# Kernel tuning notes

Measured on AMD Instinct MI355X. Metric: run time of the kernel, lower is better.

The kernel has to match this reference:

```python
import jax, jax.numpy as jnp
import numpy as np

RADIUS = 3
SIGMA = 2.0
T_STEPS = 30


def _gauss_kernel():
    i = jnp.arange(-RADIUS, RADIUS + 1, dtype=jnp.float32)
    w = jnp.exp(-0.5 * (i / SIGMA) ** 2)
    return w / w.sum()


def _gauss_axis(x, w, axis):
    # scipy mode='reflect' == numpy pad mode='symmetric'
    pad = [(0, 0)] * x.ndim
    pad[axis] = (RADIUS, RADIUS)
    xp = jnp.pad(x, pad, mode='symmetric')
    n = x.shape[axis]
    out = w[0] * jax.lax.slice_in_dim(xp, 0, n, axis=axis)
    for k in range(1, 2 * RADIUS + 1):
        out = out + w[k] * jax.lax.slice_in_dim(xp, k, k + n, axis=axis)
    return out


def _dog(x):
    # scipy gaussian_filter with scalar sigma filters EVERY axis (incl. batch, channel).
    # sigma2=0 axis filters are skipped by scipy -> blurred2 == x.
    w = _gauss_kernel()
    g = x
    for ax in range(x.ndim):
        g = _gauss_axis(g, w, ax)
    return jnp.abs(g - x)


def _conv(x, w):
    return jax.lax.conv_general_dilated(
        x, w, window_strides=(1, 1), padding='VALID',
        dimension_numbers=('NCHW', 'OIHW', 'NCHW'))


def _maxpool2(x, pad):
    return jax.lax.reduce_window(
        x, -jnp.inf, jax.lax.max, (1, 1, 2, 2), (1, 1, 2, 2),
        [(0, 0), (0, 0), (pad, pad), (pad, pad)])


def setup_inputs() -> dict:
    key = jax.random.key(0)
    kx, k1, k2, k3 = jax.random.split(key, 4)
    x = jax.random.uniform(kx, (4096, 1, 28, 28), dtype=jnp.float32)
    # model constructor takes abs() of all conv weights
    w1 = jnp.abs(jax.random.normal(k1, (4, 1, 3, 3), dtype=jnp.float32) / 3.0)
    w2 = jnp.abs(jax.random.normal(k2, (4, 4, 3, 3), dtype=jnp.float32) / 6.0)
    w3 = jnp.abs(jax.random.normal(k3, (1, 4, 3, 3), dtype=jnp.float32) / 6.0)
    return {'x': x, 'w1': w1, 'w2': w2, 'w3': w3}


def reference(x, w1, w2, w3):
    x = x.reshape(-1, 1, 28, 28)
    n = x.shape[0]
    dt = x.dtype
    # DoG preproc + global-max normalization (input is constant across timesteps,
    # so computing it once is mathematically identical to the per-step recompute)
    d = _dog(x)
    d = d / d.max()

    def step(carry, _):
        v1, v2, v3, v4, pred = carry
        # IFNode(4.5): integrate, fire, hard reset to 0
        v1 = v1 + d
        s1 = (v1 >= 4.5).astype(dt)
        v1 = jnp.where(s1 > 0, 0.0, v1)
        # conv1 -> IFNode(4.5) -> maxpool2
        v2 = v2 + _conv(s1, w1)                 # [n,4,26,26]
        s2 = (v2 >= 4.5).astype(dt)
        v2 = jnp.where(s2 > 0, 0.0, v2)
        p1 = _maxpool2(s2, 0)                   # [n,4,13,13]
        # conv2 -> IFNode(1.0) -> maxpool2(pad=1)
        v3 = v3 + _conv(p1, w2)                 # [n,4,11,11]
        s3 = (v3 >= 1.0).astype(dt)
        v3 = jnp.where(s3 > 0, 0.0, v3)
        p2 = _maxpool2(s3, 1)                   # [n,4,6,6]
        # conv3 -> LIFNode(tau=2, v_th=1.0, decay_input=True, hard reset)
        c3 = _conv(p2, w3)                      # [n,1,4,4]
        v4 = v4 + (c3 - v4) / 2.0
        s4 = (v4 >= 1.0).astype(dt)
        v4 = jnp.where(s4 > 0, 0.0, v4)
        return (v1, v2, v3, v4, pred + s4), None

    z = lambda s: jnp.zeros(s, dt)
    carry0 = (z((n, 1, 28, 28)), z((n, 4, 26, 26)), z((n, 4, 11, 11)),
              z((n, 1, 4, 4)), z((n, 1, 4, 4)))
    (v1, v2, v3, v4, pred), _ = jax.lax.scan(step, carry0, None, length=T_STEPS)
    return (pred / T_STEPS).reshape(-1, 4, 4)
```

## Files before the change

kernel.cpp:

```cpp
#include <hip/hip_runtime.h>
#include <math.h>

#define HW 784
#define TSTEPS 30
#define TCHUNK 10

struct GaussW { float w[7]; };

__device__ __forceinline__ float fadd(float a, float b) { return __fadd_rn(a, b); }
__device__ __forceinline__ float fmul(float a, float b) { return __fmul_rn(a, b); }
__device__ __forceinline__ float fsub(float a, float b) { return __fsub_rn(a, b); }

#if defined(__has_builtin)
#  if __has_builtin(__builtin_amdgcn_ubfe)
#    define UBFE(x, o, w) __builtin_amdgcn_ubfe((unsigned)(x), (unsigned)(o), (unsigned)(w))
#  endif
#endif
#ifndef UBFE
#  define UBFE(x, o, w) (((unsigned)(x) >> (o)) & ((1u << (w)) - 1u))
#endif

#define WFENCE() asm volatile("s_waitcnt lgkmcnt(0)" ::: "memory")

__device__ __forceinline__ int refl(int i, int n) {
    if (i < 0) return -i - 1;
    if (i >= n) return 2 * n - 1 - i;
    return i;
}

__device__ void dog_sample(const float* __restrict__ x, int b, int nbatch,
                           const GaussW gw, float* g, float* t,
                           float* dout, int tid) {
    for (int p = tid; p < HW; p += 256) {
        float acc = fmul(gw.w[0], x[(size_t)refl(b - 3, nbatch) * HW + p]);
        #pragma unroll
        for (int k = 1; k < 7; ++k)
            acc = fadd(acc, fmul(gw.w[k], x[(size_t)refl(b - 3 + k, nbatch) * HW + p]));
        float h = fmul(gw.w[0], acc);
        #pragma unroll
        for (int k = 1; k < 7; ++k)
            h = fadd(h, fmul(gw.w[k], acc));
        g[p] = h;
    }
    __syncthreads();
    for (int p = tid; p < HW; p += 256) {
        int i = p / 28, j = p - (p / 28) * 28;
        float acc = fmul(gw.w[0], g[refl(i - 3, 28) * 28 + j]);
        #pragma unroll
        for (int k = 1; k < 7; ++k)
            acc = fadd(acc, fmul(gw.w[k], g[refl(i - 3 + k, 28) * 28 + j]));
        t[p] = acc;
    }
    __syncthreads();
    for (int p = tid; p < HW; p += 256) {
        int i = p / 28, j = p - (p / 28) * 28;
        float acc = fmul(gw.w[0], t[i * 28 + refl(j - 3, 28)]);
        #pragma unroll
        for (int k = 1; k < 7; ++k)
            acc = fadd(acc, fmul(gw.w[k], t[i * 28 + refl(j - 3 + k, 28)]));
        dout[p] = fabsf(fsub(acc, x[(size_t)b * HW + p]));
    }
    __syncthreads();
}

__global__ void init_kernel(unsigned int* dmax) { *dmax = 0u; }

template<bool CACHE>
__global__ __launch_bounds__(256) void dmax_kernel(const float* __restrict__ x,
                                                   int nbatch, GaussW gw,
                                                   unsigned int* __restrict__ dmax,
                                                   float* __restrict__ dcache) {
    __shared__ float gS[4][HW];
    __shared__ float tS[4][HW];
    int tid = threadIdx.x;
    int lane = tid & 63, wv = tid >> 6;
    int b = blockIdx.x * 4 + wv;
    int bs = b < nbatch ? b : nbatch - 1;
    float* g = gS[wv];
    float* t = tS[wv];
    const float* xb = x + (size_t)bs * HW;
    const float* xr[7];
    #pragma unroll
    for (int k = 0; k < 7; ++k)
        xr[k] = x + (size_t)refl(bs - 3 + k, nbatch) * HW;

    for (int r = 0; r < 13; ++r) {
        int p = (r << 6) + lane;
        if (p < HW) {
            float acc = fmul(gw.w[0], xr[0][p]);
            #pragma unroll
            for (int k = 1; k < 7; ++k)
                acc = fadd(acc, fmul(gw.w[k], xr[k][p]));
            float h = fmul(gw.w[0], acc);
            #pragma unroll
            for (int k = 1; k < 7; ++k)
                h = fadd(h, fmul(gw.w[k], acc));
            g[p] = h;
        }
    }
    WFENCE();
    for (int r = 0; r < 13; ++r) {
        int p = (r << 6) + lane;
        if (p < HW) {
            int i = p / 28, j = p - (p / 28) * 28;
            float acc = fmul(gw.w[0], g[refl(i - 3, 28) * 28 + j]);
            #pragma unroll
            for (int k = 1; k < 7; ++k)
                acc = fadd(acc, fmul(gw.w[k], g[refl(i - 3 + k, 28) * 28 + j]));
            t[p] = acc;
        }
    }
    WFENCE();
    float mx = 0.f;
    for (int r = 0; r < 13; ++r) {
        int p = (r << 6) + lane;
        if (p < HW) {
            int i = p / 28, j = p - (p / 28) * 28;
            float acc = fmul(gw.w[0], t[i * 28 + refl(j - 3, 28)]);
            #pragma unroll
            for (int k = 1; k < 7; ++k)
                acc = fadd(acc, fmul(gw.w[k], t[i * 28 + refl(j - 3 + k, 28)]));
            float d = fabsf(fsub(acc, xb[p]));
            if (CACHE) dcache[(size_t)bs * HW + p] = d;
            mx = fmaxf(mx, d);
        }
    }
    #pragma unroll
    for (int off = 32; off; off >>= 1) mx = fmaxf(mx, __shfl_down(mx, off, 64));
    if (lane == 0) atomicMax(dmax, __float_as_uint(mx));
}

template<bool CACHE>
__global__ __launch_bounds__(256, 6) void sim_kernel(const float* __restrict__ x,
        int nbatch,
        const float* __restrict__ w1g, const float* __restrict__ w2g,
        const float* __restrict__ w3g, GaussW gw,
        const unsigned int* __restrict__ dmaxp,
        const float* __restrict__ dcache,
        float* __restrict__ out) {
    __shared__ __align__(16) float4 lut[512];
    __shared__ __align__(8)  float2 lut2[768];
    __shared__ float lut3[96];
    __shared__ float wts[216];
    __shared__ unsigned s1m[TCHUNK * 28];
    __shared__ unsigned p1m[TCHUNK * 52];
    __shared__ unsigned p2m[TCHUNK * 24];

    int tid = threadIdx.x;
    int b = blockIdx.x;
    if (b >= nbatch) b = nbatch - 1;

    if (tid < 36)  wts[tid]       = w1g[tid];
    if (tid < 144) wts[36 + tid]  = w2g[tid];
    if (tid < 36)  wts[180 + tid] = w3g[tid];

    float dmaxv = __uint_as_float(*dmaxp);
    float dnr[4];
    if (CACHE) {
        const float* dcb = dcache + (size_t)b * HW;
        #pragma unroll
        for (int k = 0; k < 4; ++k) {
            int p = tid + (k << 8);
            dnr[k] = (p < HW) ? __fdiv_rn(dcb[p], dmaxv) : 0.f;
        }
    } else {
        float* scr = (float*)lut;
        float* dnbuf = (float*)s1m;
        dog_sample(x, b, nbatch, gw, scr, scr + HW, dnbuf, tid);
        #pragma unroll
        for (int k = 0; k < 4; ++k) {
            int p = tid + (k << 8);
            dnr[k] = (p < HW) ? __fdiv_rn(dnbuf[p], dmaxv) : 0.f;
        }
    }
    __syncthreads();

    for (int e = tid; e < 512; e += 256) {
        float a0 = 0.f, a1 = 0.f, a2 = 0.f, a3 = 0.f;
        #pragma unroll
        for (int k = 0; k < 9; ++k) {
            bool bit = (e >> k) & 1;
            a0 = fadd(a0, bit ? wts[k]      : 0.0f);
            a1 = fadd(a1, bit ? wts[9 + k]  : 0.0f);
            a2 = fadd(a2, bit ? wts[18 + k] : 0.0f);
            a3 = fadd(a3, bit ? wts[27 + k] : 0.0f);
        }
        lut[e] = make_float4(a0, a1, a2, a3);
    }
    for (int e = tid; e < 768; e += 256) {
        int rowIdx = e >> 4, idx = e & 15;
        int cout = rowIdx / 12, rem = rowIdx - cout * 12;
        int ic = rem / 3, ki = rem - ic * 3;
        const float* wb = &wts[36 + cout * 36 + ic * 9 + ki * 3];
        float xx = 0.f, yy = 0.f;
        #pragma unroll
        for (int kk = 0; kk < 3; ++kk) {
            xx = fadd(xx, ((idx >> kk) & 1) ? wb[kk] : 0.0f);
            yy = fadd(yy, ((idx >> (kk + 1)) & 1) ? wb[kk] : 0.0f);
        }
        lut2[e] = make_float2(xx, yy);
    }
    if (tid < 96) {
        int ric = tid >> 3, idx = tid & 7;
        int ic = ric / 3, ki = ric - ic * 3;
        const float* wb = &wts[180 + ic * 9 + ki * 3];
        float xx = 0.f;
        #pragma unroll
        for (int kk = 0; kk < 3; ++kk)
            xx = fadd(xx, ((idx >> kk) & 1) ? wb[kk] : 0.0f);
        lut3[tid] = xx;
    }
    #pragma unroll
    for (int j = 0; j < 5; ++j) {
        int idx = tid + (j << 8);
        if (idx < TCHUNK * 104) {
            if (idx < 280) s1m[idx] = 0u;
            else if (idx < 800) p1m[idx - 280] = 0u;
            else p2m[idx - 800] = 0u;
        }
    }
    __syncthreads();

    int l1w_[4]; unsigned l1b_[4];
    #pragma unroll
    for (int k = 0; k < 4; ++k) {
        int e = tid + (k << 8); if (e >= HW) e = 0;
        int rw = e / 28;
        l1w_[k] = rw; l1b_[k] = 1u << (e - rw * 28);
    }
    bool okq = tid < 169;
    int qq1 = okq ? tid : 0;
    int pi1 = qq1 / 13, pj1 = qq1 - pi1 * 13;
    int sr1 = 2 * pi1; unsigned sh1 = (unsigned)(2 * pj1);
    unsigned pb1 = 1u << (pj1 + 1);
    bool hasB = tid >= 248;
    int i2cA, lb2A, p2wA; unsigned js2A, b20A, b21A;
    int i2cB, lb2B, p2wB; unsigned js2B, b20B, b21B;
    {
        int m = tid;
        int row = m / 6, sub = m - row * 6;
        int j0 = (sub < 5) ? 2 * sub : 10;
        int c = row / 11, i2 = row - c * 11;
        i2cA = i2; js2A = (unsigned)(j0 + 1); lb2A = c * 192;
        p2wA = c * 6 + ((i2 + 1) >> 1);
        b20A = 1u << (j0 >> 1);
        b21A = (sub < 5) ? (2u << (j0 >> 1)) : 0u;
        m = hasB ? 256 + (tid - 248) : 0;
        row = m / 6; sub = m - row * 6;
        j0 = (sub < 5) ? 2 * sub : 10;
        c = row / 11; i2 = row - c * 11;
        i2cB = i2; js2B = (unsigned)(j0 + 1); lb2B = c * 192;
        p2wB = c * 6 + ((i2 + 1) >> 1);
        b20B = 1u << (j0 >> 1);
        b21B = (sub < 5) ? (2u << (j0 >> 1)) : 0u;
    }
    int rr3 = (tid >> 2) & 3, cc3 = tid & 3;

    float v2q[16] = {};
    float v3A[2] = {0.f, 0.f}, v3B[2] = {0.f, 0.f};
    float v1m[4] = {};
    float v4 = 0.f, pred = 0.f;

    const float* lutf = (const float*)lut;
    (void)lutf;

    #pragma unroll 1
    for (int c = 0; c < TSTEPS / TCHUNK; ++c) {
        #pragma unroll 1
        for (int tt = 0; tt < TCHUNK; ++tt) {
            unsigned* s1 = s1m + tt * 28;
            #pragma unroll
            for (int k = 0; k < 4; ++k) {
                if (k < 3 || tid < 16) {
                    float v = fadd(v1m[k], dnr[k]);
                    bool spk = v >= 4.5f;
                    v1m[k] = spk ? 0.f : v;
                    if (spk) atomicOr(&s1[l1w_[k]], l1b_[k]);
                }
            }
        }
        __syncthreads();

        if (okq) {
            #pragma unroll 1
            for (int tt = 0; tt < TCHUNK; ++tt) {
                const unsigned* s1 = s1m + tt * 28;
                unsigned m0 = s1[sr1], m1 = s1[sr1 + 1], m2 = s1[sr1 + 2], m3 = s1[sr1 + 3];
                unsigned a = UBFE(m0, sh1, 4), bq = UBFE(m1, sh1, 4),
                         cq = UBFE(m2, sh1, 4), dq = UBFE(m3, sh1, 4);
                unsigned a7 = a & 7u, b7 = bq & 7u, c7 = cq & 7u, d7 = dq & 7u;
                unsigned a1 = a >> 1, b1 = bq >> 1, c1 = cq >> 1, d1 = dq >> 1;
                unsigned p00 = a7 | (b7 << 3) | (c7 << 6);
                unsigned p01 = a1 | (b1 << 3) | (c1 << 6);
                unsigned p10 = b7 | (c7 << 3) | (d7 << 6);
                unsigned p11 = b1 | (c1 << 3) | (d1 << 6);
                float4 e00 = lut[p00], e01 = lut[p01], e10 = lut[p10], e11 = lut[p11];
                unsigned cb0 = 0, cb1 = 0, cb2 = 0, cb3 = 0;
                #define C1U(E, ci) { float v; bool s; \
                    v = fadd(v2q[(ci)*4+0], E.x); s = v>=4.5f; v2q[(ci)*4+0] = s?0.f:v; cb0 |= (unsigned)s; \
                    v = fadd(v2q[(ci)*4+1], E.y); s = v>=4.5f; v2q[(ci)*4+1] = s?0.f:v; cb1 |= (unsigned)s; \
                    v = fadd(v2q[(ci)*4+2], E.z); s = v>=4.5f; v2q[(ci)*4+2] = s?0.f:v; cb2 |= (unsigned)s; \
                    v = fadd(v2q[(ci)*4+3], E.w); s = v>=4.5f; v2q[(ci)*4+3] = s?0.f:v; cb3 |= (unsigned)s; }
                C1U(e00, 0) C1U(e01, 1) C1U(e10, 2) C1U(e11, 3)
                #undef C1U
                unsigned* p1 = p1m + tt * 52;
                if (cb0) atomicOr(&p1[pi1],      pb1);
                if (cb1) atomicOr(&p1[13 + pi1], pb1);
                if (cb2) atomicOr(&p1[26 + pi1], pb1);
                if (cb3) atomicOr(&p1[39 + pi1], pb1);
            }
        } else {
            #pragma unroll
            for (int j = 0; j < 3; ++j) {
                int idx = (tid - 169) + 87 * j;
                if (idx < TCHUNK * 24) p2m[idx] = 0u;
            }
        }
        __syncthreads();

        #pragma unroll 1
        for (int tt = 0; tt < TCHUNK; ++tt) {
            const unsigned* p1 = p1m + tt * 52;
            unsigned* p2 = p2m + tt * 24;
            float accA = 0.f, accB = 0.f;
            #pragma unroll
            for (int ic = 0; ic < 4; ++ic)
                #pragma unroll
                for (int ki = 0; ki < 3; ++ki) {
                    unsigned row = p1[ic * 13 + i2cA + ki];
                    unsigned idx = UBFE(row, js2A, 4);
                    float2 e = lut2[lb2A + (ic * 3 + ki) * 16 + idx];
                    accA = fadd(accA, e.x);
                    accB = fadd(accB, e.y);
                }
            float va = fadd(v3A[0], accA);
            float vb = fadd(v3A[1], accB);
            bool sa = va >= 1.0f, sb = vb >= 1.0f;
            v3A[0] = sa ? 0.f : va; v3A[1] = sb ? 0.f : vb;
            unsigned orm = (sa ? b20A : 0u) | (sb ? b21A : 0u);
            if (orm) atomicOr(&p2[p2wA], orm);
        }
        if (hasB) {
            #pragma unroll 1
            for (int tt = 0; tt < TCHUNK; ++tt) {
                const unsigned* p1 = p1m + tt * 52;
                unsigned* p2 = p2m + tt * 24;
                float accA = 0.f, accB = 0.f;
                #pragma unroll
                for (int ic = 0; ic < 4; ++ic)
                    #pragma unroll
                    for (int ki = 0; ki < 3; ++ki) {
                        unsigned row = p1[ic * 13 + i2cB + ki];
                        unsigned idx = UBFE(row, js2B, 4);
                        float2 e = lut2[lb2B + (ic * 3 + ki) * 16 + idx];
                        accA = fadd(accA, e.x);
                        accB = fadd(accB, e.y);
                    }
                float va = fadd(v3B[0], accA);
                float vb = fadd(v3B[1], accB);
                bool sa = va >= 1.0f, sb = vb >= 1.0f;
                v3B[0] = sa ? 0.f : va; v3B[1] = sb ? 0.f : vb;
                unsigned orm = (sa ? b20B : 0u) | (sb ? b21B : 0u);
                if (orm) atomicOr(&p2[p2wB], orm);
            }
        }
        __syncthreads();

        if (tid < 16) {
            #pragma unroll 1
            for (int tt = 0; tt < TCHUNK; ++tt) {
                const unsigned* p2 = p2m + tt * 24;
                float acc = 0.f;
                #pragma unroll
                for (int ic = 0; ic < 4; ++ic)
                    #pragma unroll
                    for (int ki = 0; ki < 3; ++ki) {
                        unsigned row = p2[ic * 6 + rr3 + ki];
                        unsigned idx = UBFE(row, cc3, 3);
                        acc = fadd(acc, lut3[(ic * 3 + ki) * 8 + idx]);
                    }
                v4 = fadd(v4, fmul(fsub(acc, v4), 0.5f));
                if (v4 >= 1.0f) { pred += 1.f; v4 = 0.f; }
            }
        } else {
            #pragma unroll
            for (int j = 0; j < 4; ++j) {
                int idx = (tid - 16) + 240 * j;
                if (idx < 800) {
                    if (idx < 280) s1m[idx] = 0u;
                    else p1m[idx - 280] = 0u;
                }
            }
        }
        __syncthreads();
    }

    if (tid < 16 && blockIdx.x < (unsigned)nbatch)
        out[(size_t)blockIdx.x * 16 + tid] = __fdiv_rn(pred, 30.0f);
}

extern "C" void kernel_launch(void* const* d_in, const int* in_sizes, int n_in,
                              void* d_out, int out_size, void* d_ws, size_t ws_size,
                              hipStream_t stream) {
    const float* x  = (const float*)d_in[0];
    const float* w1 = (const float*)d_in[1];
    const float* w2 = (const float*)d_in[2];
    const float* w3 = (const float*)d_in[3];
    float* out = (float*)d_out;
    unsigned int* dmax = (unsigned int*)d_ws;
    float* dcache = (float*)((char*)d_ws + 16);

    int nbatch = in_sizes[0] / HW;
    size_t need = 16 + (size_t)nbatch * HW * sizeof(float);
    bool cache = ws_size >= need;
    int g4 = (nbatch + 3) / 4;

    GaussW gw;
    {
        float fw[7];
        for (int k = 0; k < 7; ++k) {
            float iv = (float)(k - 3);
            float q = iv / 2.0f;
            float e = -0.5f * (q * q);
            fw[k] = (float)exp((double)e);
        }
        float s = 0.0f;
        for (int k = 0; k < 7; ++k) s += fw[k];
        for (int k = 0; k < 7; ++k) gw.w[k] = fw[k] / s;
    }

    hipLaunchKernelGGL(init_kernel, dim3(1), dim3(1), 0, stream, dmax);
    if (cache) {
        hipLaunchKernelGGL(dmax_kernel<true>, dim3(g4), dim3(256), 0, stream,
                           x, nbatch, gw, dmax, dcache);
        hipLaunchKernelGGL(sim_kernel<true>, dim3(nbatch), dim3(256), 0, stream,
                           x, nbatch, w1, w2, w3, gw, dmax, dcache, out);
    } else {
        hipLaunchKernelGGL(dmax_kernel<false>, dim3(g4), dim3(256), 0, stream,
                           x, nbatch, gw, dmax, dcache);
        hipLaunchKernelGGL(sim_kernel<false>, dim3(nbatch), dim3(256), 0, stream,
                           x, nbatch, w1, w2, w3, gw, dmax, dcache, out);
    }
}
```

Before: 269.4 us.

## Pack pooled spike maps two channels per word and compute conv2 with register weights

Pooled layer-1 and layer-2 spike bitmaps are repacked so two (layer-1) or four (layer-2) channels share one 32-bit word, which reduces shared-memory words, zeroing work and the number of atomicOr operations. Conv2 drops the lut2 table lookups and instead keeps each thread's 36 output-channel weights in registers, selecting each weight with a sign-extended bit mask and AND. Work is redistributed so every thread handles 1-3 output cells, which removes the separate second pass for threads 248-255. The register-held weights raise register pressure, and launch bounds are lowered from 6 to 5 blocks per CU to allow for that.

```diff
diff --git a/kernel.cpp b/kernel.cpp
--- a/kernel.cpp
+++ b/kernel.cpp
@@ -12,13 +12,21 @@
 __device__ __forceinline__ float fsub(float a, float b) { return __fsub_rn(a, b); }
 
 #if defined(__has_builtin)
+#  if __has_builtin(__builtin_amdgcn_sbfe)
+#    define SBFE(x, b) __builtin_amdgcn_sbfe((int)(x), (unsigned)(b), 1u)
+#  endif
 #  if __has_builtin(__builtin_amdgcn_ubfe)
 #    define UBFE(x, o, w) __builtin_amdgcn_ubfe((unsigned)(x), (unsigned)(o), (unsigned)(w))
 #  endif
 #endif
+#ifndef SBFE
+#  define SBFE(x, b) (((int)((unsigned)(x) << (31 - (b)))) >> 31)
+#endif
 #ifndef UBFE
 #  define UBFE(x, o, w) (((unsigned)(x) >> (o)) & ((1u << (w)) - 1u))
 #endif
+
+#define SELW(rw, b, w) __int_as_float(SBFE((rw), (b)) & __float_as_int(w))
 
 #define WFENCE() asm volatile("s_waitcnt lgkmcnt(0)" ::: "memory")
 
@@ -131,7 +139,7 @@
 }
 
 template<bool CACHE>
-__global__ __launch_bounds__(256, 6) void sim_kernel(const float* __restrict__ x,
+__global__ __launch_bounds__(256, 5) void sim_kernel(const float* __restrict__ x,
         int nbatch,
         const float* __restrict__ w1g, const float* __restrict__ w2g,
         const float* __restrict__ w3g, GaussW gw,
@@ -139,12 +147,11 @@
         const float* __restrict__ dcache,
         float* __restrict__ out) {
     __shared__ __align__(16) float4 lut[512];
-    __shared__ __align__(8)  float2 lut2[768];
     __shared__ float lut3[96];
     __shared__ float wts[216];
     __shared__ unsigned s1m[TCHUNK * 28];
-    __shared__ unsigned p1m[TCHUNK * 52];
-    __shared__ unsigned p2m[TCHUNK * 24];
+    __shared__ unsigned p1p[TCHUNK * 26];
+    __shared__ unsigned p2p[TCHUNK * 6];
 
     int tid = threadIdx.x;
     int b = blockIdx.x;
@@ -165,12 +172,11 @@
         }
     } else {
         float* scr = (float*)lut;
-        float* dnbuf = (float*)s1m;
-        dog_sample(x, b, nbatch, gw, scr, scr + HW, dnbuf, tid);
+        dog_sample(x, b, nbatch, gw, scr, scr + HW, scr, tid);
         #pragma unroll
         for (int k = 0; k < 4; ++k) {
             int p = tid + (k << 8);
-            dnr[k] = (p < HW) ? __fdiv_rn(dnbuf[p], dmaxv) : 0.f;
+            dnr[k] = (p < HW) ? __fdiv_rn(scr[p], dmaxv) : 0.f;
         }
     }
     __syncthreads();
@@ -187,19 +193,6 @@
         }
         lut[e] = make_float4(a0, a1, a2, a3);
     }
-    for (int e = tid; e < 768; e += 256) {
-        int rowIdx = e >> 4, idx = e & 15;
-        int cout = rowIdx / 12, rem = rowIdx - cout * 12;
-        int ic = rem / 3, ki = rem - ic * 3;
-        const float* wb = &wts[36 + cout * 36 + ic * 9 + ki * 3];
-        float xx = 0.f, yy = 0.f;
-        #pragma unroll
-        for (int kk = 0; kk < 3; ++kk) {
-            xx = fadd(xx, ((idx >> kk) & 1) ? wb[kk] : 0.0f);
-            yy = fadd(yy, ((idx >> (kk + 1)) & 1) ? wb[kk] : 0.0f);
-        }
-        lut2[e] = make_float2(xx, yy);
-    }
     if (tid < 96) {
         int ric = tid >> 3, idx = tid & 7;
         int ic = ric / 3, ki = ric - ic * 3;
@@ -211,12 +204,12 @@
         lut3[tid] = xx;
     }
     #pragma unroll
-    for (int j = 0; j < 5; ++j) {
+    for (int j = 0; j < 3; ++j) {
         int idx = tid + (j << 8);
-        if (idx < TCHUNK * 104) {
+        if (idx < 600) {
             if (idx < 280) s1m[idx] = 0u;
-            else if (idx < 800) p1m[idx - 280] = 0u;
-            else p2m[idx - 800] = 0u;
+            else if (idx < 540) p1p[idx - 280] = 0u;
+            else p2p[idx - 540] = 0u;
         }
     }
     __syncthreads();
@@ -233,36 +226,33 @@
     int pi1 = qq1 / 13, pj1 = qq1 - pi1 * 13;
     int sr1 = 2 * pi1; unsigned sh1 = (unsigned)(2 * pj1);
     unsigned pb1 = 1u << (pj1 + 1);
-    bool hasB = tid >= 248;
-    int i2cA, lb2A, p2wA; unsigned js2A, b20A, b21A;
-    int i2cB, lb2B, p2wB; unsigned js2B, b20B, b21B;
+    int c2, i2, jp0, ncell2;
     {
-        int m = tid;
-        int row = m / 6, sub = m - row * 6;
-        int j0 = (sub < 5) ? 2 * sub : 10;
-        int c = row / 11, i2 = row - c * 11;
-        i2cA = i2; js2A = (unsigned)(j0 + 1); lb2A = c * 192;
-        p2wA = c * 6 + ((i2 + 1) >> 1);
-        b20A = 1u << (j0 >> 1);
-        b21A = (sub < 5) ? (2u << (j0 >> 1)) : 0u;
-        m = hasB ? 256 + (tid - 248) : 0;
-        row = m / 6; sub = m - row * 6;
-        j0 = (sub < 5) ? 2 * sub : 10;
-        c = row / 11; i2 = row - c * 11;
-        i2cB = i2; js2B = (unsigned)(j0 + 1); lb2B = c * 192;
-        p2wB = c * 6 + ((i2 + 1) >> 1);
-        b20B = 1u << (j0 >> 1);
-        b21B = (sub < 5) ? (2u << (j0 >> 1)) : 0u;
-    }
+        int rowid, sub;
+        if (tid < 216) {
+            rowid = tid / 6; sub = tid - rowid * 6;
+            jp0 = (sub < 5) ? 2 * sub : 10; ncell2 = (sub < 5) ? 2 : 1;
+        } else {
+            int u = tid - 216; int r5 = u / 5; sub = u - r5 * 5;
+            rowid = 36 + r5;
+            jp0 = (sub < 4) ? 2 * sub : 8; ncell2 = (sub < 4) ? 2 : 3;
+        }
+        c2 = rowid / 11; i2 = rowid - c2 * 11;
+    }
+    unsigned js2 = (unsigned)(jp0 + 1);
+    int shf6 = 6 * c2;
+    int p2row = (i2 + 1) >> 1;
+    unsigned bA = 1u << (jp0 >> 1), bB = 2u << (jp0 >> 1);
     int rr3 = (tid >> 2) & 3, cc3 = tid & 3;
 
+    float w2r[36];
+    #pragma unroll
+    for (int m = 0; m < 36; ++m) w2r[m] = wts[36 + c2 * 36 + m];
+
     float v2q[16] = {};
-    float v3A[2] = {0.f, 0.f}, v3B[2] = {0.f, 0.f};
+    float v3m[3] = {0.f, 0.f, 0.f};
     float v1m[4] = {};
     float v4 = 0.f, pred = 0.f;
-
-    const float* lutf = (const float*)lut;
-    (void)lutf;
 
     #pragma unroll 1
     for (int c = 0; c < TSTEPS / TCHUNK; ++c) {
@@ -303,92 +293,95 @@
                     v = fadd(v2q[(ci)*4+3], E.w); s = v>=4.5f; v2q[(ci)*4+3] = s?0.f:v; cb3 |= (unsigned)s; }
                 C1U(e00, 0) C1U(e01, 1) C1U(e10, 2) C1U(e11, 3)
                 #undef C1U
-                unsigned* p1 = p1m + tt * 52;
-                if (cb0) atomicOr(&p1[pi1],      pb1);
-                if (cb1) atomicOr(&p1[13 + pi1], pb1);
-                if (cb2) atomicOr(&p1[26 + pi1], pb1);
-                if (cb3) atomicOr(&p1[39 + pi1], pb1);
+                unsigned* pw = &p1p[(tt * 13 + pi1) * 2];
+                unsigned orm0 = (cb0 ? pb1 : 0u) | (cb1 ? (pb1 << 16) : 0u);
+                unsigned orm1 = (cb2 ? pb1 : 0u) | (cb3 ? (pb1 << 16) : 0u);
+                if (orm0) atomicOr(&pw[0], orm0);
+                if (orm1) atomicOr(&pw[1], orm1);
             }
         } else {
-            #pragma unroll
-            for (int j = 0; j < 3; ++j) {
-                int idx = (tid - 169) + 87 * j;
-                if (idx < TCHUNK * 24) p2m[idx] = 0u;
-            }
+            int idx = tid - 169;
+            if (idx < TCHUNK * 6) p2p[idx] = 0u;
         }
         __syncthreads();
 
         #pragma unroll 1
         for (int tt = 0; tt < TCHUNK; ++tt) {
-            const unsigned* p1 = p1m + tt * 52;
-            unsigned* p2 = p2m + tt * 24;
-            float accA = 0.f, accB = 0.f;
-            #pragma unroll
-            for (int ic = 0; ic < 4; ++ic)
+            const unsigned* pp = &p1p[tt * 26];
+            unsigned wq0 = pp[(i2 + 0) * 2], wq0b = pp[(i2 + 0) * 2 + 1];
+            unsigned wq1 = pp[(i2 + 1) * 2], wq1b = pp[(i2 + 1) * 2 + 1];
+            unsigned wq2 = pp[(i2 + 2) * 2], wq2b = pp[(i2 + 2) * 2 + 1];
+            float a0 = 0.f, a1 = 0.f, a2 = 0.f;
+            #pragma unroll
+            for (int ic = 0; ic < 4; ++ic) {
+                unsigned w0r = (ic < 2) ? wq0 : wq0b;
+                unsigned w1r = (ic < 2) ? wq1 : wq1b;
+                unsigned w2w = (ic < 2) ? wq2 : wq2b;
+                unsigned sh = js2 + ((ic & 1) << 4);
                 #pragma unroll
                 for (int ki = 0; ki < 3; ++ki) {
-                    unsigned row = p1[ic * 13 + i2cA + ki];
-                    unsigned idx = UBFE(row, js2A, 4);
-                    float2 e = lut2[lb2A + (ic * 3 + ki) * 16 + idx];
-                    accA = fadd(accA, e.x);
-                    accB = fadd(accB, e.y);
+                    unsigned rw = ((ki == 0) ? w0r : (ki == 1) ? w1r : w2w) >> sh;
+                    int w0 = __float_as_int(w2r[ic * 9 + ki * 3 + 0]);
+                    int w1 = __float_as_int(w2r[ic * 9 + ki * 3 + 1]);
+                    int w2i = __float_as_int(w2r[ic * 9 + ki * 3 + 2]);
+                    int m0 = SBFE(rw, 0), m1 = SBFE(rw, 1), m2 = SBFE(rw, 2);
+                    a0 = fadd(a0, __int_as_float(m0 & w0));
+                    a0 = fadd(a0, __int_as_float(m1 & w1));
+                    a0 = fadd(a0, __int_as_float(m2 & w2i));
+                    if (ncell2 >= 2) {
+                        int m3 = SBFE(rw, 3);
+                        a1 = fadd(a1, __int_as_float(m1 & w0));
+                        a1 = fadd(a1, __int_as_float(m2 & w1));
+                        a1 = fadd(a1, __int_as_float(m3 & w2i));
+                        if (ncell2 == 3) {
+                            int m4 = SBFE(rw, 4);
+                            a2 = fadd(a2, __int_as_float(m2 & w0));
+                            a2 = fadd(a2, __int_as_float(m3 & w1));
+                            a2 = fadd(a2, __int_as_float(m4 & w2i));
+                        }
+                    }
                 }
-            float va = fadd(v3A[0], accA);
-            float vb = fadd(v3A[1], accB);
-            bool sa = va >= 1.0f, sb = vb >= 1.0f;
-            v3A[0] = sa ? 0.f : va; v3A[1] = sb ? 0.f : vb;
-            unsigned orm = (sa ? b20A : 0u) | (sb ? b21A : 0u);
-            if (orm) atomicOr(&p2[p2wA], orm);
-        }
-        if (hasB) {
-            #pragma unroll 1
-            for (int tt = 0; tt < TCHUNK; ++tt) {
-                const unsigned* p1 = p1m + tt * 52;
-                unsigned* p2 = p2m + tt * 24;
-                float accA = 0.f, accB = 0.f;
-                #pragma unroll
-                for (int ic = 0; ic < 4; ++ic)
-                    #pragma unroll
-                    for (int ki = 0; ki < 3; ++ki) {
-                        unsigned row = p1[ic * 13 + i2cB + ki];
-                        unsigned idx = UBFE(row, js2B, 4);
-                        float2 e = lut2[lb2B + (ic * 3 + ki) * 16 + idx];
-                        accA = fadd(accA, e.x);
-                        accB = fadd(accB, e.y);
-                    }
-                float va = fadd(v3B[0], accA);
-                float vb = fadd(v3B[1], accB);
-                bool sa = va >= 1.0f, sb = vb >= 1.0f;
-                v3B[0] = sa ? 0.f : va; v3B[1] = sb ? 0.f : vb;
-                unsigned orm = (sa ? b20B : 0u) | (sb ? b21B : 0u);
-                if (orm) atomicOr(&p2[p2wB], orm);
-            }
+            }
+            unsigned orm = 0u;
+            { float v = fadd(v3m[0], a0); bool s = v >= 1.0f;
+              v3m[0] = s ? 0.f : v; if (s) orm |= bA; }
+            if (ncell2 >= 2) {
+                float v = fadd(v3m[1], a1); bool s = v >= 1.0f;
+                v3m[1] = s ? 0.f : v; if (s) orm |= bB;
+                if (ncell2 == 3) {
+                    float v2 = fadd(v3m[2], a2); bool s2 = v2 >= 1.0f;
+                    v3m[2] = s2 ? 0.f : v2; if (s2) orm |= bB;
+                }
+            }
+            if (orm) atomicOr(&p2p[tt * 6 + p2row], orm << shf6);
         }
         __syncthreads();
 
         if (tid < 16) {
             #pragma unroll 1
             for (int tt = 0; tt < TCHUNK; ++tt) {
-                const unsigned* p2 = p2m + tt * 24;
+                const unsigned* p2 = &p2p[tt * 6];
+                unsigned r0 = p2[rr3], r1 = p2[rr3 + 1], r2 = p2[rr3 + 2];
                 float acc = 0.f;
                 #pragma unroll
-                for (int ic = 0; ic < 4; ++ic)
+                for (int ic = 0; ic < 4; ++ic) {
                     #pragma unroll
                     for (int ki = 0; ki < 3; ++ki) {
-                        unsigned row = p2[ic * 6 + rr3 + ki];
-                        unsigned idx = UBFE(row, cc3, 3);
+                        unsigned row = (ki == 0) ? r0 : (ki == 1) ? r1 : r2;
+                        unsigned idx = UBFE(row, 6 * ic + cc3, 3);
                         acc = fadd(acc, lut3[(ic * 3 + ki) * 8 + idx]);
                     }
+                }
                 v4 = fadd(v4, fmul(fsub(acc, v4), 0.5f));
                 if (v4 >= 1.0f) { pred += 1.f; v4 = 0.f; }
             }
         } else {
             #pragma unroll
-            for (int j = 0; j < 4; ++j) {
+            for (int j = 0; j < 3; ++j) {
                 int idx = (tid - 16) + 240 * j;
-                if (idx < 800) {
+                if (idx < 540) {
                     if (idx < 280) s1m[idx] = 0u;
-                    else p1m[idx - 280] = 0u;
+                    else p1p[idx - 280] = 0u;
                 }
             }
         }
```

New measurement: 639.2 us. 137% more time.

## Pack pooled spike bitmasks across channels into shared words

Applied to the files above, without the earlier changes.

Repacks the pooled spike bitmaps so that two channels share one 32-bit word per row for pool1, stored as uint2 pairs, and all four channels share one word per row for pool2. Conv2 and conv3 threads now load three packed rows and extract bits per channel with shifted bitfield extracts, instead of issuing twelve separate shared-memory loads. The A and B conv2 loops are merged into one time loop, and the DoG scratch buffer moves so it no longer aliases s1m. This cuts LDS loads, atomic ORs and zeroing work, at the cost of more atomic contention per word and some leftover dead code.

```diff
diff --git a/kernel.cpp b/kernel.cpp
--- a/kernel.cpp
+++ b/kernel.cpp
@@ -143,8 +143,8 @@
     __shared__ float lut3[96];
     __shared__ float wts[216];
     __shared__ unsigned s1m[TCHUNK * 28];
-    __shared__ unsigned p1m[TCHUNK * 52];
-    __shared__ unsigned p2m[TCHUNK * 24];
+    __shared__ __align__(8) unsigned p1p[TCHUNK * 26];
+    __shared__ unsigned p2p[TCHUNK * 6];
 
     int tid = threadIdx.x;
     int b = blockIdx.x;
@@ -165,12 +165,11 @@
         }
     } else {
         float* scr = (float*)lut;
-        float* dnbuf = (float*)s1m;
-        dog_sample(x, b, nbatch, gw, scr, scr + HW, dnbuf, tid);
+        dog_sample(x, b, nbatch, gw, scr, scr + HW, scr, tid);
         #pragma unroll
         for (int k = 0; k < 4; ++k) {
             int p = tid + (k << 8);
-            dnr[k] = (p < HW) ? __fdiv_rn(dnbuf[p], dmaxv) : 0.f;
+            dnr[k] = (p < HW) ? __fdiv_rn(scr[p], dmaxv) : 0.f;
         }
     }
     __syncthreads();
@@ -211,12 +210,12 @@
         lut3[tid] = xx;
     }
     #pragma unroll
-    for (int j = 0; j < 5; ++j) {
+    for (int j = 0; j < 3; ++j) {
         int idx = tid + (j << 8);
-        if (idx < TCHUNK * 104) {
+        if (idx < 600) {
             if (idx < 280) s1m[idx] = 0u;
-            else if (idx < 800) p1m[idx - 280] = 0u;
-            else p2m[idx - 800] = 0u;
+            else if (idx < 540) p1p[idx - 280] = 0u;
+            else p2p[idx - 540] = 0u;
         }
     }
     __syncthreads();
@@ -234,35 +233,39 @@
     int sr1 = 2 * pi1; unsigned sh1 = (unsigned)(2 * pj1);
     unsigned pb1 = 1u << (pj1 + 1);
     bool hasB = tid >= 248;
-    int i2cA, lb2A, p2wA; unsigned js2A, b20A, b21A;
-    int i2cB, lb2B, p2wB; unsigned js2B, b20B, b21B;
+    int i2cA, lb2A, p2wA; unsigned js2A, shA, b20A, b21A;
+    int i2cB, lb2B, p2wB; unsigned js2B, shB, b20B, b21B;
     {
         int m = tid;
         int row = m / 6, sub = m - row * 6;
         int j0 = (sub < 5) ? 2 * sub : 10;
         int c = row / 11, i2 = row - c * 11;
-        i2cA = i2; js2A = (unsigned)(j0 + 1); lb2A = c * 192;
-        p2wA = c * 6 + ((i2 + 1) >> 1);
+        i2cA = i2; js2A = (unsigned)(j0 + 1) + ((unsigned)(c & 1) << 4);
+        lb2A = c * 192; shA = 6u * (unsigned)c;
+        p2wA = (i2 + 1) >> 1;
         b20A = 1u << (j0 >> 1);
         b21A = (sub < 5) ? (2u << (j0 >> 1)) : 0u;
+        int wA = c >> 1; i2cA = i2cA * 2 + wA;
+        i2cA = i2;
         m = hasB ? 256 + (tid - 248) : 0;
         row = m / 6; sub = m - row * 6;
         j0 = (sub < 5) ? 2 * sub : 10;
         c = row / 11; i2 = row - c * 11;
-        i2cB = i2; js2B = (unsigned)(j0 + 1); lb2B = c * 192;
-        p2wB = c * 6 + ((i2 + 1) >> 1);
+        i2cB = i2; js2B = (unsigned)(j0 + 1) + ((unsigned)(c & 1) << 4);
+        lb2B = c * 192; shB = 6u * (unsigned)c;
+        p2wB = (i2 + 1) >> 1;
         b20B = 1u << (j0 >> 1);
         b21B = (sub < 5) ? (2u << (j0 >> 1)) : 0u;
     }
+    int cwA = 0, cwB = 0;
+    { int m = tid; int row = m / 6; cwA = (row / 11) >> 1; }
+    { int m = hasB ? 256 + (tid - 248) : 0; int row = m / 6; cwB = (row / 11) >> 1; }
     int rr3 = (tid >> 2) & 3, cc3 = tid & 3;
 
     float v2q[16] = {};
     float v3A[2] = {0.f, 0.f}, v3B[2] = {0.f, 0.f};
     float v1m[4] = {};
     float v4 = 0.f, pred = 0.f;
-
-    const float* lutf = (const float*)lut;
-    (void)lutf;
 
     #pragma unroll 1
     for (int c = 0; c < TSTEPS / TCHUNK; ++c) {
@@ -303,65 +306,74 @@
                     v = fadd(v2q[(ci)*4+3], E.w); s = v>=4.5f; v2q[(ci)*4+3] = s?0.f:v; cb3 |= (unsigned)s; }
                 C1U(e00, 0) C1U(e01, 1) C1U(e10, 2) C1U(e11, 3)
                 #undef C1U
-                unsigned* p1 = p1m + tt * 52;
-                if (cb0) atomicOr(&p1[pi1],      pb1);
-                if (cb1) atomicOr(&p1[13 + pi1], pb1);
-                if (cb2) atomicOr(&p1[26 + pi1], pb1);
-                if (cb3) atomicOr(&p1[39 + pi1], pb1);
+                unsigned* pw = &p1p[(tt * 13 + pi1) * 2];
+                unsigned orm0 = (cb0 ? pb1 : 0u) | (cb1 ? (pb1 << 16) : 0u);
+                unsigned orm1 = (cb2 ? pb1 : 0u) | (cb3 ? (pb1 << 16) : 0u);
+                if (orm0) atomicOr(&pw[0], orm0);
+                if (orm1) atomicOr(&pw[1], orm1);
             }
         } else {
-            #pragma unroll
-            for (int j = 0; j < 3; ++j) {
-                int idx = (tid - 169) + 87 * j;
-                if (idx < TCHUNK * 24) p2m[idx] = 0u;
-            }
+            int idx = tid - 169;
+            if (idx < TCHUNK * 6) p2p[idx] = 0u;
         }
         __syncthreads();
 
         #pragma unroll 1
         for (int tt = 0; tt < TCHUNK; ++tt) {
-            const unsigned* p1 = p1m + tt * 52;
-            unsigned* p2 = p2m + tt * 24;
-            float accA = 0.f, accB = 0.f;
-            #pragma unroll
-            for (int ic = 0; ic < 4; ++ic)
-                #pragma unroll
-                for (int ki = 0; ki < 3; ++ki) {
-                    unsigned row = p1[ic * 13 + i2cA + ki];
-                    unsigned idx = UBFE(row, js2A, 4);
-                    float2 e = lut2[lb2A + (ic * 3 + ki) * 16 + idx];
-                    accA = fadd(accA, e.x);
-                    accB = fadd(accB, e.y);
-                }
-            float va = fadd(v3A[0], accA);
-            float vb = fadd(v3A[1], accB);
-            bool sa = va >= 1.0f, sb = vb >= 1.0f;
-            v3A[0] = sa ? 0.f : va; v3A[1] = sb ? 0.f : vb;
-            unsigned orm = (sa ? b20A : 0u) | (sb ? b21A : 0u);
-            if (orm) atomicOr(&p2[p2wA], orm);
-        }
-        if (hasB) {
-            #pragma unroll 1
-            for (int tt = 0; tt < TCHUNK; ++tt) {
-                const unsigned* p1 = p1m + tt * 52;
-                unsigned* p2 = p2m + tt * 24;
+            const uint2* pp = (const uint2*)&p1p[tt * 26];
+            unsigned* p2w = &p2p[tt * 6];
+            {
+                uint2 r0 = pp[i2cA], r1 = pp[i2cA + 1], r2 = pp[i2cA + 2];
                 float accA = 0.f, accB = 0.f;
                 #pragma unroll
-                for (int ic = 0; ic < 4; ++ic)
+                for (int ic = 0; ic < 4; ++ic) {
+                    unsigned w0 = (cwA == 0) ? ((ic < 2) ? r0.x : r0.y)
+                                             : ((ic < 2) ? r0.x : r0.y);
+                    unsigned rw0 = (ic < 2) ? r0.x : r0.y;
+                    unsigned rw1 = (ic < 2) ? r1.x : r1.y;
+                    unsigned rw2 = (ic < 2) ? r2.x : r2.y;
+                    unsigned fo = (unsigned)(js2A & 15u) + ((unsigned)(ic & 1) << 4);
+                    (void)w0;
                     #pragma unroll
                     for (int ki = 0; ki < 3; ++ki) {
-                        unsigned row = p1[ic * 13 + i2cB + ki];
-                        unsigned idx = UBFE(row, js2B, 4);
+                        unsigned row = (ki == 0) ? rw0 : (ki == 1) ? rw1 : rw2;
+                        unsigned idx = UBFE(row, fo, 4);
+                        float2 e = lut2[lb2A + (ic * 3 + ki) * 16 + idx];
+                        accA = fadd(accA, e.x);
+                        accB = fadd(accB, e.y);
+                    }
+                }
+                float va = fadd(v3A[0], accA);
+                float vb = fadd(v3A[1], accB);
+                bool sa = va >= 1.0f, sb = vb >= 1.0f;
+                v3A[0] = sa ? 0.f : va; v3A[1] = sb ? 0.f : vb;
+                unsigned orm = (sa ? b20A : 0u) | (sb ? b21A : 0u);
+                if (orm) atomicOr(&p2w[p2wA], orm << shA);
+            }
+            if (hasB) {
+                uint2 r0 = pp[i2cB], r1 = pp[i2cB + 1], r2 = pp[i2cB + 2];
+                float accA = 0.f, accB = 0.f;
+                #pragma unroll
+                for (int ic = 0; ic < 4; ++ic) {
+                    unsigned rw0 = (ic < 2) ? r0.x : r0.y;
+                    unsigned rw1 = (ic < 2) ? r1.x : r1.y;
+                    unsigned rw2 = (ic < 2) ? r2.x : r2.y;
+                    unsigned fo = (unsigned)(js2B & 15u) + ((unsigned)(ic & 1) << 4);
+                    #pragma unroll
+                    for (int ki = 0; ki < 3; ++ki) {
+                        unsigned row = (ki == 0) ? rw0 : (ki == 1) ? rw1 : rw2;
+                        unsigned idx = UBFE(row, fo, 4);
                         float2 e = lut2[lb2B + (ic * 3 + ki) * 16 + idx];
                         accA = fadd(accA, e.x);
                         accB = fadd(accB, e.y);
                     }
+                }
                 float va = fadd(v3B[0], accA);
                 float vb = fadd(v3B[1], accB);
                 bool sa = va >= 1.0f, sb = vb >= 1.0f;
                 v3B[0] = sa ? 0.f : va; v3B[1] = sb ? 0.f : vb;
                 unsigned orm = (sa ? b20B : 0u) | (sb ? b21B : 0u);
-                if (orm) atomicOr(&p2[p2wB], orm);
+                if (orm) atomicOr(&p2w[p2wB], orm << shB);
             }
         }
         __syncthreads();
@@ -369,26 +381,28 @@
         if (tid < 16) {
             #pragma unroll 1
             for (int tt = 0; tt < TCHUNK; ++tt) {
-                const unsigned* p2 = p2m + tt * 24;
+                const unsigned* p2 = &p2p[tt * 6];
+                unsigned r0 = p2[rr3], r1 = p2[rr3 + 1], r2 = p2[rr3 + 2];
                 float acc = 0.f;
                 #pragma unroll
-                for (int ic = 0; ic < 4; ++ic)
+                for (int ic = 0; ic < 4; ++ic) {
                     #pragma unroll
                     for (int ki = 0; ki < 3; ++ki) {
-                        unsigned row = p2[ic * 6 + rr3 + ki];
-                        unsigned idx = UBFE(row, cc3, 3);
+                        unsigned row = (ki == 0) ? r0 : (ki == 1) ? r1 : r2;
+                        unsigned idx = UBFE(row, 6 * ic + cc3, 3);
                         acc = fadd(acc, lut3[(ic * 3 + ki) * 8 + idx]);
                     }
+                }
                 v4 = fadd(v4, fmul(fsub(acc, v4), 0.5f));
                 if (v4 >= 1.0f) { pred += 1.f; v4 = 0.f; }
             }
         } else {
             #pragma unroll
-            for (int j = 0; j < 4; ++j) {
+            for (int j = 0; j < 3; ++j) {
                 int idx = (tid - 16) + 240 * j;
-                if (idx < 800) {
+                if (idx < 540) {
                     if (idx < 280) s1m[idx] = 0u;
-                    else p1m[idx - 280] = 0u;
+                    else p1p[idx - 280] = 0u;
                 }
             }
         }
```

New measurement: 273.2 us. Within noise of the previous version (+1.4%).
